# Kernel tuning notes

Hardware: AMD Instinct MI355X
Metric: run time of the kernel (lower is better)

## Reference

```python
import jax, jax.numpy as jnp
import numpy as np

B, L, C, H = 2, 4096, 1024, 16
D = C // H
KERNEL_FROM_KN = lambda kn: int(np.sqrt(kn)) + 1


def setup_inputs() -> dict:
    key = jax.random.key(0)
    ks = jax.random.split(key, 4)
    s = 0.02
    kk = KERNEL_FROM_KN(144)  # 13
    return {
        "x": jax.random.normal(ks[0], (B, L, C), jnp.float32),
        "w_qkv": jax.random.normal(ks[1], (C, 3 * C), jnp.float32) * s,
        "b_qkv": jnp.zeros((3 * C,), jnp.float32),
        "rpb": jax.random.normal(ks[2], (H, 2 * kk - 1), jnp.float32) * s,
        "w_proj": jax.random.normal(ks[3], (C, C), jnp.float32) * s,
        "b_proj": jnp.zeros((C,), jnp.float32),
        "k_neighbors": 144,
    }


def reference(x, w_qkv, b_qkv, rpb, w_proj, b_proj, k_neighbors):
    kk = KERNEL_FROM_KN(k_neighbors)  # kernel size (13)
    scale = D ** -0.5
    qkv = (x @ w_qkv + b_qkv).reshape(B, L, 3, H, D).transpose(2, 0, 3, 1, 4)  # (3,B,H,L,D)
    q, k, v = qkv[0] * scale, qkv[1], qkv[2]
    pos = jnp.arange(L)
    # NATTEN window: centered, clamped so the full kernel fits inside [0, L)
    start = jnp.clip(pos - kk // 2, 0, L - kk)               # (L,)
    idx = start[:, None] + jnp.arange(kk)[None, :]           # (L,kk) key positions
    k_win = k[:, :, idx, :]                                  # (B,H,L,kk,D)
    v_win = v[:, :, idx, :]                                  # (B,H,L,kk,D)
    attn = jnp.einsum('bhld,bhlkd->bhlk', q, k_win)          # (B,H,L,kk)
    # relative-position bias index = key_pos - query_pos + (kk - 1) in [0, 2kk-2]
    bias_idx = idx - pos[:, None] + (kk - 1)                 # (L,kk)
    attn = attn + rpb[:, bias_idx][None]                     # broadcast over batch
    attn = jax.nn.softmax(attn, axis=-1)
    out = jnp.einsum('bhlk,bhlkd->bhld', attn, v_win)        # (B,H,L,D)
    out = out.transpose(0, 2, 1, 3).reshape(B, L, C)
    return out @ w_proj + b_proj
```

## Files before the change

### kernel.cpp

```cpp
#include <hip/hip_runtime.h>
#include <hip/hip_bf16.h>
#include <stdint.h>

typedef __bf16 bf16x8 __attribute__((ext_vector_type(8)));
typedef float floatx4 __attribute__((ext_vector_type(4)));

#define B_ 2
#define L_ 4096
#define C_ 1024
#define H_ 16
#define D_ 64
constexpr size_t TEN = (size_t)B_ * H_ * L_ * D_;
#define LOG2E 1.4426950408889634f

__device__ __forceinline__ float bf2f(unsigned short u) {
  union { unsigned int i; float f; } x; x.i = ((unsigned int)u) << 16; return x.f;
}
__device__ __forceinline__ float exp2fast(float x) {
  return __builtin_amdgcn_exp2f(x);
}

__device__ __forceinline__ void async_copy16(const unsigned short* g, unsigned short* l) {
  __builtin_amdgcn_global_load_lds(
      (const __attribute__((address_space(1))) unsigned int*)g,
      (__attribute__((address_space(3))) unsigned int*)l,
      16, 0, 0);
}

__global__ __launch_bounds__(256) void cvt_f32_bf16_kernel(
    const float* __restrict__ in, unsigned short* __restrict__ out, int n) {
  int i = (blockIdx.x * 256 + threadIdx.x) * 8;
  if (i >= n) return;
  float4 a = *(const float4*)&in[i];
  float4 b = *(const float4*)&in[i + 4];
  union { uint4 u; __bf16 h[8]; } st;
  st.h[0] = (__bf16)a.x; st.h[1] = (__bf16)a.y; st.h[2] = (__bf16)a.z; st.h[3] = (__bf16)a.w;
  st.h[4] = (__bf16)b.x; st.h[5] = (__bf16)b.y; st.h[6] = (__bf16)b.z; st.h[7] = (__bf16)b.w;
  *(uint4*)&out[i] = st.u;
}

__global__ __launch_bounds__(256) void transpose_f32_bf16(
    const float* __restrict__ in, unsigned short* __restrict__ out,
    int R, int Ccols) {
  __shared__ float tile[64][65];
  const int bx = blockIdx.x * 64;
  const int by = blockIdx.y * 64;
  const int t = threadIdx.x;
  for (int i = t; i < 1024; i += 256) {
    int r = i >> 4, c4 = (i & 15) << 2;
    float4 v = *(const float4*)&in[(size_t)(by + r) * Ccols + bx + c4];
    tile[r][c4] = v.x; tile[r][c4 + 1] = v.y; tile[r][c4 + 2] = v.z; tile[r][c4 + 3] = v.w;
  }
  __syncthreads();
  for (int i = t; i < 512; i += 256) {
    int r = i >> 3, c8 = (i & 7) << 3;
    union { uint4 u; __bf16 h[8]; } st;
    #pragma unroll
    for (int j = 0; j < 8; ++j) st.h[j] = (__bf16)tile[c8 + j][r];
    *(uint4*)&out[(size_t)(bx + r) * R + by + c8] = st.u;
  }
}

template <int MODE>
__global__ __launch_bounds__(256) void gemm_bt_kernel(
    const unsigned short* __restrict__ A, const unsigned short* __restrict__ Bt,
    const float* __restrict__ bias, unsigned short* __restrict__ out_bf,
    float* __restrict__ out_f, int M, int N, int K, float qscale) {
  constexpr int BK = 64;
  __shared__ unsigned short a_sh[128 * BK];
  __shared__ unsigned short b_sh[128 * BK];

  const int t = threadIdx.x;
  const int nwgx = gridDim.x;
  const int nwg = nwgx * gridDim.y;
  const int flat = blockIdx.y * nwgx + blockIdx.x;
  const int cpx = nwg >> 3;
  const int swz = (flat & 7) * cpx + (flat >> 3);
  const int n0 = (swz % nwgx) * 128;
  const int m0 = (swz / nwgx) * 128;

  const int wave = t >> 6, lane = t & 63;
  const int wr = wave >> 1, wc = wave & 1;
  const int lm = lane & 15, quad = lane >> 4;

  const int soff = t * 8;
  const int srow = soff >> 6;
  const int scol = soff & 63;

  floatx4 acc[4][4];
  #pragma unroll
  for (int i = 0; i < 4; ++i)
    #pragma unroll
    for (int j = 0; j < 4; ++j) acc[i][j] = (floatx4)0.0f;

  for (int kt = 0; kt < K; kt += BK) {
    #pragma unroll
    for (int p = 0; p < 4; ++p) {
      int r = srow + p * 32;
      int c = scol ^ ((r & 7) << 3);
      int off = r * BK + scol;
      async_copy16(&A[(size_t)(m0 + r) * K + kt + c], &a_sh[off]);
      async_copy16(&Bt[(size_t)(n0 + r) * K + kt + c], &b_sh[off]);
    }
    __syncthreads();
    #pragma unroll
    for (int ks = 0; ks < BK; ks += 32) {
      bf16x8 af[4], bfr[4];
      #pragma unroll
      for (int i = 0; i < 4; ++i) {
        int ra = wr * 64 + i * 16 + lm;
        af[i] = *(const bf16x8*)&a_sh[ra * BK + ((ks + quad * 8) ^ ((ra & 7) << 3))];
      }
      #pragma unroll
      for (int j = 0; j < 4; ++j) {
        int rb = wc * 64 + j * 16 + lm;
        bfr[j] = *(const bf16x8*)&b_sh[rb * BK + ((ks + quad * 8) ^ ((rb & 7) << 3))];
      }
      #pragma unroll
      for (int i = 0; i < 4; ++i)
        #pragma unroll
        for (int j = 0; j < 4; ++j)
          acc[i][j] = __builtin_amdgcn_mfma_f32_16x16x32_bf16(af[i], bfr[j], acc[i][j], 0, 0, 0);
    }
    __syncthreads();
  }

  #pragma unroll
  for (int j = 0; j < 4; ++j) {
    int col = n0 + wc * 64 + j * 16 + lm;
    float bv = bias[col];
    if (MODE == 0) {
      int h = col >> 6, d = col & 63;
      #pragma unroll
      for (int i = 0; i < 4; ++i)
        #pragma unroll
        for (int r = 0; r < 4; ++r) {
          int row = m0 + wr * 64 + i * 16 + quad * 4 + r;
          int b = row >> 12, l = row & (L_ - 1);
          float v = (acc[i][j][r] + bv) * qscale;
          ((__bf16*)out_bf)[((size_t)(b * H_ + h) * L_ + l) * D_ + d] = (__bf16)v;
        }
    } else {
      #pragma unroll
      for (int i = 0; i < 4; ++i)
        #pragma unroll
        for (int r = 0; r < 4; ++r) {
          int row = m0 + wr * 64 + i * 16 + quad * 4 + r;
          out_f[(size_t)row * N + col] = acc[i][j][r] + bv;
        }
    }
  }
}

constexpr int KKMAX = 63;
constexpr int TL = 128;
constexpr int LDK = 72;

__global__ __launch_bounds__(256) void natt_kernel(
    const unsigned short* __restrict__ qkv,
    const float* __restrict__ rpb,
    const int* __restrict__ knp,
    unsigned short* __restrict__ attn_out) {
  __shared__ unsigned short k_sh[(TL + KKMAX) * LDK];
  __shared__ unsigned short v_sh[(TL + KKMAX) * LDK];
  __shared__ float rpb_sh[2 * KKMAX + 1];

  const int bh = blockIdx.x;
  const int h = bh & (H_ - 1);
  const int b = bh >> 4;
  const int l0 = blockIdx.y * TL;
  const int t = threadIdx.x;

  int kn = knp[0];
  if (kn > 65536 || kn < 0) {
    union { int i; float f; } u; u.i = kn; kn = (int)u.f;
  }
  int rr = 1;
  while ((rr + 1) * (rr + 1) <= kn) ++rr;
  int kk = rr + 1;
  if (kk > KKMAX) kk = KKMAX;

  int base = l0 - kk / 2;
  if (base < 0) base = 0;
  if (base > L_ - kk) base = L_ - kk;
  int nrows = TL + kk;
  if (nrows > L_ - base) nrows = L_ - base;

  const unsigned short* kg = qkv + TEN + (size_t)bh * L_ * D_;
  const unsigned short* vg = qkv + 2 * TEN + (size_t)bh * L_ * D_;

  for (int i = t; i < nrows * 8; i += 256) {
    int row = i >> 3, c8 = (i & 7) << 3;
    uint4 kv = *(const uint4*)&kg[(size_t)(base + row) * D_ + c8];
    *(uint4*)&k_sh[row * LDK + c8] = kv;
    uint4 vv = *(const uint4*)&vg[(size_t)(base + row) * D_ + c8];
    *(uint4*)&v_sh[row * LDK + c8] = vv;
  }
  int nb = 2 * kk - 1;
  for (int i = t; i < nb; i += 256) rpb_sh[i] = rpb[h * nb + i] * LOG2E;
  __syncthreads();

  const int qi = t >> 1, half = t & 1;
  const int l = l0 + qi;

  const unsigned short* qg = qkv + (size_t)bh * L_ * D_ + (size_t)l * D_ + half * 32;
  float qv[32];
  #pragma unroll
  for (int c = 0; c < 4; ++c) {
    union { uint4 u; unsigned short s[8]; } ld;
    ld.u = *(const uint4*)&qg[c * 8];
    #pragma unroll
    for (int j = 0; j < 8; ++j) qv[c * 8 + j] = bf2f(ld.s[j]);
  }

  int start = l - kk / 2;
  if (start < 0) start = 0;
  if (start > L_ - kk) start = L_ - kk;
  const int srow = start - base;
  const int boff = start - l + kk - 1;

  float m = -1e30f, lsum = 0.0f;
  float accv[32];
  #pragma unroll
  for (int d = 0; d < 32; ++d) accv[d] = 0.0f;

  for (int j = 0; j < kk; ++j) {
    const unsigned short* kr = &k_sh[(srow + j) * LDK + half * 32];
    float partial = 0.0f;
    #pragma unroll
    for (int c = 0; c < 4; ++c) {
      union { uint4 u; unsigned short s[8]; } ld;
      ld.u = *(const uint4*)&kr[c * 8];
      #pragma unroll
      for (int jj = 0; jj < 8; ++jj) partial += qv[c * 8 + jj] * bf2f(ld.s[jj]);
    }
    float s = partial + __shfl_xor(partial, 1) + rpb_sh[boff + j];
    float p;
    if (s - m > 8.0f) {
      float corr = exp2fast(m - s);
      lsum *= corr;
      #pragma unroll
      for (int d = 0; d < 32; ++d) accv[d] *= corr;
      m = s;
      p = 1.0f;
    } else {
      p = exp2fast(s - m);
    }
    lsum += p;
    const unsigned short* vr = &v_sh[(srow + j) * LDK + half * 32];
    #pragma unroll
    for (int c = 0; c < 4; ++c) {
      union { uint4 u; unsigned short s[8]; } ld;
      ld.u = *(const uint4*)&vr[c * 8];
      #pragma unroll
      for (int jj = 0; jj < 8; ++jj) accv[c * 8 + jj] += p * bf2f(ld.s[jj]);
    }
  }
  float inv = 1.0f / lsum;
  unsigned short* og = attn_out + ((size_t)(b * L_ + l) * C_ + h * D_ + half * 32);
  #pragma unroll
  for (int c = 0; c < 4; ++c) {
    union { uint4 u; __bf16 h8[8]; } st;
    #pragma unroll
    for (int jj = 0; jj < 8; ++jj) st.h8[jj] = (__bf16)(accv[c * 8 + jj] * inv);
    *(uint4*)&og[c * 8] = st.u;
  }
}

extern "C" void kernel_launch(void* const* d_in, const int* in_sizes, int n_in,
                              void* d_out, int out_size, void* d_ws, size_t ws_size,
                              hipStream_t stream) {
  const float* x      = (const float*)d_in[0];
  const float* w_qkv  = (const float*)d_in[1];
  const float* b_qkv  = (const float*)d_in[2];
  const float* rpb    = (const float*)d_in[3];
  const float* w_proj = (const float*)d_in[4];
  const float* b_proj = (const float*)d_in[5];
  const int* kn       = (const int*)d_in[6];
  float* out          = (float*)d_out;

  unsigned short* ws      = (unsigned short*)d_ws;
  unsigned short* wT_qkv  = ws;
  unsigned short* wT_proj = wT_qkv + (size_t)3072 * 1024;
  unsigned short* x_bf    = wT_proj + (size_t)1024 * 1024;
  unsigned short* qkv_ws  = x_bf + (size_t)8192 * 1024;
  unsigned short* attn_ws = qkv_ws + 3 * TEN;

  cvt_f32_bf16_kernel<<<(8192 * 1024) / (256 * 8), 256, 0, stream>>>(x, x_bf, 8192 * 1024);
  transpose_f32_bf16<<<dim3(3072 / 64, 1024 / 64), 256, 0, stream>>>(w_qkv, wT_qkv, 1024, 3072);
  transpose_f32_bf16<<<dim3(1024 / 64, 1024 / 64), 256, 0, stream>>>(w_proj, wT_proj, 1024, 1024);
  gemm_bt_kernel<0><<<dim3(1024 / 128, 8192 / 128), 256, 0, stream>>>(
      x_bf, wT_qkv, b_qkv, qkv_ws, nullptr,
      8192, 1024, 1024, 0.125f * LOG2E);
  gemm_bt_kernel<0><<<dim3(1024 / 128, 8192 / 128), 256, 0, stream>>>(
      x_bf, wT_qkv + (size_t)1024 * 1024, b_qkv + 1024, qkv_ws + TEN, nullptr,
      8192, 1024, 1024, 1.0f);
  gemm_bt_kernel<0><<<dim3(1024 / 128, 8192 / 128), 256, 0, stream>>>(
      x_bf, wT_qkv + (size_t)2048 * 1024, b_qkv + 2048, qkv_ws + 2 * TEN, nullptr,
      8192, 1024, 1024, 1.0f);
  natt_kernel<<<dim3(B_ * H_, L_ / TL), 256, 0, stream>>>(qkv_ws, rpb, kn, attn_ws);
  gemm_bt_kernel<1><<<dim3(1024 / 128, 8192 / 128), 256, 0, stream>>>(
      attn_ws, wT_proj, b_proj, nullptr, out, 8192, 1024, 1024, 1.0f);
}
```

Before: 229.1 us.

## Fuse x fp32-to-bf16 conversion into a single merged QKV GEMM

Removes the separate x conversion kernel. The QKV GEMM now loads fp32 x directly, converting it to bf16 in registers and storing it to padded LDS. The three Q/K/V GEMM launches are merged into one N=3072 launch, which routes each column to its Q, K or V slice and applies the Q scale only to Q columns. This avoids writing and re-reading the bf16 copy of x and cuts launches. In exchange, the A-tile load becomes synchronous global-to-register-to-LDS instead of async, and x tiles are reconverted by every column block.

```diff
diff --git a/kernel.cpp b/kernel.cpp
--- a/kernel.cpp
+++ b/kernel.cpp
@@ -25,18 +25,6 @@
       (const __attribute__((address_space(1))) unsigned int*)g,
       (__attribute__((address_space(3))) unsigned int*)l,
       16, 0, 0);
-}
-
-__global__ __launch_bounds__(256) void cvt_f32_bf16_kernel(
-    const float* __restrict__ in, unsigned short* __restrict__ out, int n) {
-  int i = (blockIdx.x * 256 + threadIdx.x) * 8;
-  if (i >= n) return;
-  float4 a = *(const float4*)&in[i];
-  float4 b = *(const float4*)&in[i + 4];
-  union { uint4 u; __bf16 h[8]; } st;
-  st.h[0] = (__bf16)a.x; st.h[1] = (__bf16)a.y; st.h[2] = (__bf16)a.z; st.h[3] = (__bf16)a.w;
-  st.h[4] = (__bf16)b.x; st.h[5] = (__bf16)b.y; st.h[6] = (__bf16)b.z; st.h[7] = (__bf16)b.w;
-  *(uint4*)&out[i] = st.u;
 }
 
 __global__ __launch_bounds__(256) void transpose_f32_bf16(
@@ -61,13 +49,14 @@
   }
 }
 
-template <int MODE>
+template <int MODE, bool AF32>
 __global__ __launch_bounds__(256) void gemm_bt_kernel(
-    const unsigned short* __restrict__ A, const unsigned short* __restrict__ Bt,
+    const void* __restrict__ Av, const unsigned short* __restrict__ Bt,
     const float* __restrict__ bias, unsigned short* __restrict__ out_bf,
     float* __restrict__ out_f, int M, int N, int K, float qscale) {
   constexpr int BK = 64;
-  __shared__ unsigned short a_sh[128 * BK];
+  constexpr int LDA = 72;
+  __shared__ unsigned short a_sh[128 * LDA];
   __shared__ unsigned short b_sh[128 * BK];
 
   const int t = threadIdx.x;
@@ -83,24 +72,46 @@
   const int wr = wave >> 1, wc = wave & 1;
   const int lm = lane & 15, quad = lane >> 4;
 
-  const int soff = t * 8;
-  const int srow = soff >> 6;
-  const int scol = soff & 63;
+  const int srow = t >> 3;
+  const int scol = (t & 7) * 8;
 
   floatx4 acc[4][4];
   #pragma unroll
   for (int i = 0; i < 4; ++i)
     #pragma unroll
     for (int j = 0; j < 4; ++j) acc[i][j] = (floatx4)0.0f;
+
+  const float* Af = (const float*)Av;
+  const unsigned short* Ab = (const unsigned short*)Av;
 
   for (int kt = 0; kt < K; kt += BK) {
     #pragma unroll
     for (int p = 0; p < 4; ++p) {
       int r = srow + p * 32;
       int c = scol ^ ((r & 7) << 3);
-      int off = r * BK + scol;
-      async_copy16(&A[(size_t)(m0 + r) * K + kt + c], &a_sh[off]);
-      async_copy16(&Bt[(size_t)(n0 + r) * K + kt + c], &b_sh[off]);
+      async_copy16(&Bt[(size_t)(n0 + r) * K + kt + c], &b_sh[r * BK + scol]);
+    }
+    if (AF32) {
+      #pragma unroll
+      for (int p = 0; p < 4; ++p) {
+        int r = srow + p * 32;
+        const float* src = &Af[(size_t)(m0 + r) * K + kt + scol];
+        float4 v0 = *(const float4*)src;
+        float4 v1 = *(const float4*)(src + 4);
+        union { uint4 u; __bf16 h[8]; } st;
+        st.h[0] = (__bf16)v0.x; st.h[1] = (__bf16)v0.y;
+        st.h[2] = (__bf16)v0.z; st.h[3] = (__bf16)v0.w;
+        st.h[4] = (__bf16)v1.x; st.h[5] = (__bf16)v1.y;
+        st.h[6] = (__bf16)v1.z; st.h[7] = (__bf16)v1.w;
+        *(uint4*)&a_sh[r * LDA + scol] = st.u;
+      }
+    } else {
+      #pragma unroll
+      for (int p = 0; p < 4; ++p) {
+        int r = srow + p * 32;
+        int c = scol ^ ((r & 7) << 3);
+        async_copy16(&Ab[(size_t)(m0 + r) * K + kt + c], &a_sh[r * BK + scol]);
+      }
     }
     __syncthreads();
     #pragma unroll
@@ -109,7 +120,10 @@
       #pragma unroll
       for (int i = 0; i < 4; ++i) {
         int ra = wr * 64 + i * 16 + lm;
-        af[i] = *(const bf16x8*)&a_sh[ra * BK + ((ks + quad * 8) ^ ((ra & 7) << 3))];
+        if (AF32)
+          af[i] = *(const bf16x8*)&a_sh[ra * LDA + ks + quad * 8];
+        else
+          af[i] = *(const bf16x8*)&a_sh[ra * BK + ((ks + quad * 8) ^ ((ra & 7) << 3))];
       }
       #pragma unroll
       for (int j = 0; j < 4; ++j) {
@@ -130,15 +144,18 @@
     int col = n0 + wc * 64 + j * 16 + lm;
     float bv = bias[col];
     if (MODE == 0) {
-      int h = col >> 6, d = col & 63;
+      int which = col >> 10;
+      int rem = col & 1023;
+      int h = rem >> 6, d = rem & 63;
+      float mul = (which == 0) ? qscale : 1.0f;
       #pragma unroll
       for (int i = 0; i < 4; ++i)
         #pragma unroll
         for (int r = 0; r < 4; ++r) {
           int row = m0 + wr * 64 + i * 16 + quad * 4 + r;
           int b = row >> 12, l = row & (L_ - 1);
-          float v = (acc[i][j][r] + bv) * qscale;
-          ((__bf16*)out_bf)[((size_t)(b * H_ + h) * L_ + l) * D_ + d] = (__bf16)v;
+          float v = (acc[i][j][r] + bv) * mul;
+          ((__bf16*)out_bf)[(size_t)which * TEN + (((size_t)(b * H_ + h) * L_ + l) * D_ + d)] = (__bf16)v;
         }
     } else {
       #pragma unroll
@@ -282,23 +299,14 @@
   unsigned short* ws      = (unsigned short*)d_ws;
   unsigned short* wT_qkv  = ws;
   unsigned short* wT_proj = wT_qkv + (size_t)3072 * 1024;
-  unsigned short* x_bf    = wT_proj + (size_t)1024 * 1024;
-  unsigned short* qkv_ws  = x_bf + (size_t)8192 * 1024;
+  unsigned short* qkv_ws  = wT_proj + (size_t)1024 * 1024;
   unsigned short* attn_ws = qkv_ws + 3 * TEN;
 
-  cvt_f32_bf16_kernel<<<(8192 * 1024) / (256 * 8), 256, 0, stream>>>(x, x_bf, 8192 * 1024);
   transpose_f32_bf16<<<dim3(3072 / 64, 1024 / 64), 256, 0, stream>>>(w_qkv, wT_qkv, 1024, 3072);
   transpose_f32_bf16<<<dim3(1024 / 64, 1024 / 64), 256, 0, stream>>>(w_proj, wT_proj, 1024, 1024);
-  gemm_bt_kernel<0><<<dim3(1024 / 128, 8192 / 128), 256, 0, stream>>>(
-      x_bf, wT_qkv, b_qkv, qkv_ws, nullptr,
-      8192, 1024, 1024, 0.125f * LOG2E);
-  gemm_bt_kernel<0><<<dim3(1024 / 128, 8192 / 128), 256, 0, stream>>>(
-      x_bf, wT_qkv + (size_t)1024 * 1024, b_qkv + 1024, qkv_ws + TEN, nullptr,
-      8192, 1024, 1024, 1.0f);
-  gemm_bt_kernel<0><<<dim3(1024 / 128, 8192 / 128), 256, 0, stream>>>(
-      x_bf, wT_qkv + (size_t)2048 * 1024, b_qkv + 2048, qkv_ws + 2 * TEN, nullptr,
-      8192, 1024, 1024, 1.0f);
+  gemm_bt_kernel<0, true><<<dim3(3072 / 128, 8192 / 128), 256, 0, stream>>>(
+      x, wT_qkv, b_qkv, qkv_ws, nullptr, 8192, 3072, 1024, 0.125f * LOG2E);
   natt_kernel<<<dim3(B_ * H_, L_ / TL), 256, 0, stream>>>(qkv_ws, rpb, kn, attn_ws);
-  gemm_bt_kernel<1><<<dim3(1024 / 128, 8192 / 128), 256, 0, stream>>>(
+  gemm_bt_kernel<1, false><<<dim3(1024 / 128, 8192 / 128), 256, 0, stream>>>(
       attn_ws, wT_proj, b_proj, nullptr, out, 8192, 1024, 1024, 1.0f);
 }
```

After: 244.2 us. +6.6%, slower.
